# Kernel tuning notes

Hardware: AMD Instinct MI355X
Metric: run time of the kernel (lower is better)

## Reference

```python
import jax, jax.numpy as jnp
import numpy as np


def setup_inputs() -> dict:
    key = jax.random.key(0)
    x = jax.random.normal(key, (4, 4, 32, 256, 256), dtype=jnp.float32)
    return {"x": x}


def reference(x):
    # NonMaximaSuppression3d with kernel_size=(3,3,3) fast path:
    # a voxel survives iff it is strictly greater than all 26 neighbors;
    # border voxels (no full neighborhood) are always suppressed.
    B, CH, D, H, W = x.shape
    ct = x[..., 1:-1, 1:-1, 1:-1]  # interior centers [B,CH,D-2,H-2,W-2]
    mask_inner = jnp.ones(ct.shape, dtype=bool)
    for dz in range(3):
        for dy in range(3):
            for dx in range(3):
                if (dz, dy, dx) == (1, 1, 1):
                    continue
                neigh = x[..., dz:D - 2 + dz, dy:H - 2 + dy, dx:W - 2 + dx]
                mask_inner = mask_inner & (ct > neigh)
    mask = jnp.zeros(x.shape, dtype=bool).at[..., 1:-1, 1:-1, 1:-1].set(mask_inner)
    return x * mask.astype(x.dtype)
```

## Files before the change

### kernel.cpp

```cpp
#include <hip/hip_runtime.h>


typedef float v4f __attribute__((ext_vector_type(4)));

constexpr int W  = 256;
constexpr int H  = 256;
constexpr int D  = 32;
constexpr int SH = W;
constexpr int SD = W * H;
constexpr int KD = 4;
constexpr int HC = 4;
constexpr int BC = 16;
constexpr int DG = D / KD;
constexpr int HG = H / HC;
constexpr int NPL = KD + 2;
constexpr int NR  = HC + 2;
constexpr int TROWS = NPL * NR;

__device__ __forceinline__ v4f vmax4(v4f a, v4f b) {
    return (v4f){fmaxf(a.x, b.x), fmaxf(a.y, b.y), fmaxf(a.z, b.z), fmaxf(a.w, b.w)};
}

__global__ __launch_bounds__(256, 4) void nms3d_kernel(const float* __restrict__ x,
                                                       float* __restrict__ out) {
    __shared__ float lds[TROWS * W];

    const int blk  = blockIdx.x;
    const int wv   = threadIdx.x >> 6;
    const int lane = threadIdx.x & 63;
    const int hc   = blk & (HG - 1);
    const int dg   = (blk >> 6) & (DG - 1);
    const int bc   = blk >> 9;
    const int d0   = dg * KD;
    const int h0   = hc * HC;

    const float* vol = x + bc * (D * SD);

    #pragma unroll
    for (int u = 0; u < TROWS / 4; ++u) {
        const int t = wv * (TROWS / 4) + u;
        const int j = t / NR;
        const int r = t - j * NR;
        int p = d0 - 1 + j;  p = p < 0 ? 0 : (p > D - 1 ? D - 1 : p);
        int hh = h0 - 1 + r; hh = hh < 0 ? 0 : (hh > H - 1 ? H - 1 : hh);
        const float* gp = vol + p * SD + hh * SH + (lane << 2);
        __builtin_amdgcn_global_load_lds(
            (const __attribute__((address_space(1))) unsigned int*)gp,
            (__attribute__((address_space(3))) unsigned int*)&lds[(j * NR + r) * W],
            16, 0, 0);
    }
    __syncthreads();

    const int d = d0 + wv;
    const bool dv = (d > 0) && (d < D - 1);
    float* ovol = out + bc * (D * SD) + d * SD + (lane << 2);

    const float* Lm = lds + (wv * NR) * W + (lane << 2);
    const float* L0 = lds + ((wv + 1) * NR) * W + (lane << 2);
    const float* Lp = lds + ((wv + 2) * NR) * W + (lane << 2);

    v4f rm[3], r0[3], rp[3];
    rm[0] = *(const v4f*)(Lm + 0 * W); r0[0] = *(const v4f*)(L0 + 0 * W); rp[0] = *(const v4f*)(Lp + 0 * W);
    rm[1] = *(const v4f*)(Lm + 1 * W); r0[1] = *(const v4f*)(L0 + 1 * W); rp[1] = *(const v4f*)(Lp + 1 * W);

    #pragma unroll
    for (int i = 0; i < HC; ++i) {
        const int s0 = i % 3, s1 = (i + 1) % 3, s2 = (i + 2) % 3;
        rm[s2] = *(const v4f*)(Lm + (i + 2) * W);
        r0[s2] = *(const v4f*)(L0 + (i + 2) * W);
        rp[s2] = *(const v4f*)(Lp + (i + 2) * W);

        const v4f a3m = vmax4(vmax4(rm[s0], rm[s1]), rm[s2]);
        const v4f a3p = vmax4(vmax4(rp[s0], rp[s1]), rp[s2]);
        const v4f a20 = vmax4(r0[s0], r0[s2]);
        const v4f v8  = vmax4(vmax4(a3m, a3p), a20);
        const v4f c   = r0[s1];

        const float l8 = __shfl_up(v8.w, 1);
        const float r8 = __shfl_down(v8.x, 1);
        const float lc = __shfl_up(c.w, 1);
        const float rc = __shfl_down(c.x, 1);

        float n0 = fmaxf(fmaxf(l8,   v8.x), v8.y);
        float n1 = fmaxf(fmaxf(v8.x, v8.y), v8.z);
        float n2 = fmaxf(fmaxf(v8.y, v8.z), v8.w);
        float n3 = fmaxf(fmaxf(v8.z, v8.w), r8);
        n0 = fmaxf(n0, fmaxf(lc,  c.y));
        n1 = fmaxf(n1, fmaxf(c.x, c.z));
        n2 = fmaxf(n2, fmaxf(c.y, c.w));
        n3 = fmaxf(n3, fmaxf(c.z, rc));

        const int h = h0 + i;
        const bool hv = (h > 0) && (h < H - 1);
        const bool v  = hv && dv;
        v4f o;
        o.x = (v && lane > 0  && c.x > n0) ? c.x : 0.f;
        o.y = (v && c.y > n1) ? c.y : 0.f;
        o.z = (v && c.z > n2) ? c.z : 0.f;
        o.w = (v && lane < 63 && c.w > n3) ? c.w : 0.f;
        __builtin_nontemporal_store(o, (v4f*)(ovol + h * SH));
    }
}

extern "C" void kernel_launch(void* const* d_in, const int* in_sizes, int n_in,
                              void* d_out, int out_size, void* d_ws, size_t ws_size,
                              hipStream_t stream) {
    const float* x = (const float*)d_in[0];
    float* out = (float*)d_out;
    const int grid = BC * DG * HG;
    nms3d_kernel<<<grid, 256, 0, stream>>>(x, out);
}
```

Measured before the change: 222.8 us.

## Replace LDS staging with direct global loads and taller per-wave row strips

```diff
diff --git a/kernel.cpp b/kernel.cpp
--- a/kernel.cpp
+++ b/kernel.cpp
@@ -8,14 +8,12 @@
 constexpr int D  = 32;
 constexpr int SH = W;
 constexpr int SD = W * H;
-constexpr int KD = 4;
-constexpr int HC = 4;
+constexpr int KD  = 4;
+constexpr int HCW = 16;
 constexpr int BC = 16;
 constexpr int DG = D / KD;
-constexpr int HG = H / HC;
-constexpr int NPL = KD + 2;
-constexpr int NR  = HC + 2;
-constexpr int TROWS = NPL * NR;
+constexpr int HG = H / HCW;
+constexpr int NWG = BC * DG * HG;
 
 __device__ __forceinline__ v4f vmax4(v4f a, v4f b) {
     return (v4f){fmaxf(a.x, b.x), fmaxf(a.y, b.y), fmaxf(a.z, b.z), fmaxf(a.w, b.w)};
@@ -23,52 +21,46 @@
 
 __global__ __launch_bounds__(256, 4) void nms3d_kernel(const float* __restrict__ x,
                                                        float* __restrict__ out) {
-    __shared__ float lds[TROWS * W];
-
     const int blk  = blockIdx.x;
     const int wv   = threadIdx.x >> 6;
     const int lane = threadIdx.x & 63;
-    const int hc   = blk & (HG - 1);
-    const int dg   = (blk >> 6) & (DG - 1);
-    const int bc   = blk >> 9;
-    const int d0   = dg * KD;
-    const int h0   = hc * HC;
+    const int hg   = blk & (HG - 1);
+    const int dg   = (blk >> 4) & (DG - 1);
+    const int bc   = blk >> 7;
+    const int d    = dg * KD + wv;
+    const int h0   = hg * HCW;
 
     const float* vol = x + bc * (D * SD);
+    const int pm = d == 0     ? 0     : d - 1;
+    const int pp = d == D - 1 ? D - 1 : d + 1;
+    const int om = pm * SD + (lane << 2);
+    const int o0 = d  * SD + (lane << 2);
+    const int op = pp * SD + (lane << 2);
 
-    #pragma unroll
-    for (int u = 0; u < TROWS / 4; ++u) {
-        const int t = wv * (TROWS / 4) + u;
-        const int j = t / NR;
-        const int r = t - j * NR;
-        int p = d0 - 1 + j;  p = p < 0 ? 0 : (p > D - 1 ? D - 1 : p);
-        int hh = h0 - 1 + r; hh = hh < 0 ? 0 : (hh > H - 1 ? H - 1 : hh);
-        const float* gp = vol + p * SD + hh * SH + (lane << 2);
-        __builtin_amdgcn_global_load_lds(
-            (const __attribute__((address_space(1))) unsigned int*)gp,
-            (__attribute__((address_space(3))) unsigned int*)&lds[(j * NR + r) * W],
-            16, 0, 0);
-    }
-    __syncthreads();
-
-    const int d = d0 + wv;
     const bool dv = (d > 0) && (d < D - 1);
     float* ovol = out + bc * (D * SD) + d * SD + (lane << 2);
 
-    const float* Lm = lds + (wv * NR) * W + (lane << 2);
-    const float* L0 = lds + ((wv + 1) * NR) * W + (lane << 2);
-    const float* Lp = lds + ((wv + 2) * NR) * W + (lane << 2);
-
-    v4f rm[3], r0[3], rp[3];
-    rm[0] = *(const v4f*)(Lm + 0 * W); r0[0] = *(const v4f*)(L0 + 0 * W); rp[0] = *(const v4f*)(Lp + 0 * W);
-    rm[1] = *(const v4f*)(Lm + 1 * W); r0[1] = *(const v4f*)(L0 + 1 * W); rp[1] = *(const v4f*)(Lp + 1 * W);
+    v4f rm[4], r0[4], rp[4];
 
     #pragma unroll
-    for (int i = 0; i < HC; ++i) {
-        const int s0 = i % 3, s1 = (i + 1) % 3, s2 = (i + 2) % 3;
-        rm[s2] = *(const v4f*)(Lm + (i + 2) * W);
-        r0[s2] = *(const v4f*)(L0 + (i + 2) * W);
-        rp[s2] = *(const v4f*)(Lp + (i + 2) * W);
+    for (int r = 0; r < 3; ++r) {
+        int hh = h0 - 1 + r; hh = hh < 0 ? 0 : hh;
+        const int o = hh * SH;
+        rm[r] = *(const v4f*)(vol + om + o);
+        r0[r] = *(const v4f*)(vol + o0 + o);
+        rp[r] = *(const v4f*)(vol + op + o);
+    }
+
+    #pragma unroll
+    for (int i = 0; i < HCW; ++i) {
+        if (i + 3 <= HCW + 1) {
+            int hh = h0 - 1 + (i + 3); hh = hh > H - 1 ? H - 1 : hh;
+            const int o = hh * SH, s = (i + 3) & 3;
+            rm[s] = *(const v4f*)(vol + om + o);
+            r0[s] = *(const v4f*)(vol + o0 + o);
+            rp[s] = *(const v4f*)(vol + op + o);
+        }
+        const int s0 = i & 3, s1 = (i + 1) & 3, s2 = (i + 2) & 3;
 
         const v4f a3m = vmax4(vmax4(rm[s0], rm[s1]), rm[s2]);
         const v4f a3p = vmax4(vmax4(rp[s0], rp[s1]), rp[s2]);
@@ -107,6 +99,5 @@
                               hipStream_t stream) {
     const float* x = (const float*)d_in[0];
     float* out = (float*)d_out;
-    const int grid = BC * DG * HG;
-    nms3d_kernel<<<grid, 256, 0, stream>>>(x, out);
+    nms3d_kernel<<<NWG, 256, 0, stream>>>(x, out);
 }
```

Result: slower. 232.6 us (+4.4%).
